# Optimization experiments

Hardware: AMD Instinct MI355X
Metric: run time of the kernel (lower is better)

The kernel has to match this reference:

```python
import jax, jax.numpy as jnp
import numpy as np

H = 8            # heads
M = 256          # num_landmarks
PINV_ITERS = 6
PAD = 16         # residual_conv_kernel(33)//2


def layernorm(x, g, b, eps=1e-5):
    mu = x.mean(-1, keepdims=True)
    var = ((x - mu) ** 2).mean(-1, keepdims=True)
    return (x - mu) * jax.lax.rsqrt(var + eps) * g + b


def moore_penrose_pinv(x, iters=PINV_ITERS):
    # iterative Moore-Penrose pseudo-inverse (Nystromformer)
    abs_x = jnp.abs(x)
    col = abs_x.sum(-1)
    row = abs_x.sum(-2)
    z = jnp.swapaxes(x, -1, -2) / (jnp.max(col) * jnp.max(row))
    eye = jnp.eye(x.shape[-1], dtype=x.dtype)
    for _ in range(iters):
        xz = x @ z
        z = 0.25 * z @ (13.0 * eye - xz @ (15.0 * eye - xz @ (7.0 * eye - xz)))
    return z


def attn_block(y, ln1_g, ln1_b, w_qkv, w_out, b_out, res_w,
               ln2_g, ln2_b, w1, b1, w2, b2):
    B, N, D = y.shape
    inner = w_qkv.shape[1] // 3
    dh = inner // H
    xn = layernorm(y, ln1_g, ln1_b)
    qkv = xn @ w_qkv                      # [B,N,3*inner]
    q, k, v = jnp.split(qkv, 3, axis=-1)
    to_heads = lambda t: t.reshape(B, N, H, dh).transpose(0, 2, 1, 3)  # [B,H,N,dh]
    q, k, v = map(to_heads, (q, k, v))
    q = q * (dh ** -0.5)
    l = N // M                            # tokens per landmark (N % M == 0 here)
    q_l = q.reshape(B, H, M, l, dh).mean(3)  # sum/l == mean -> [B,H,M,dh]
    k_l = k.reshape(B, H, M, l, dh).mean(3)
    attn1 = jax.nn.softmax(jnp.einsum('bhnd,bhmd->bhnm', q, k_l), axis=-1)
    attn2 = jax.nn.softmax(jnp.einsum('bhid,bhjd->bhij', q_l, k_l), axis=-1)
    attn3 = jax.nn.softmax(jnp.einsum('bhmd,bhnd->bhmn', q_l, k), axis=-1)
    attn2_inv = moore_penrose_pinv(attn2)
    out = (attn1 @ attn2_inv) @ (attn3 @ v)   # [B,H,N,dh]
    # depthwise residual conv over sequence dim: v as NCHW with C=H, Hdim=N, Wdim=dh
    res = jax.lax.conv_general_dilated(
        v, res_w, window_strides=(1, 1), padding=[(PAD, PAD), (0, 0)],
        dimension_numbers=('NCHW', 'OIHW', 'NCHW'), feature_group_count=H)
    out = out + res
    out = out.transpose(0, 2, 1, 3).reshape(B, N, inner)
    y = y + out @ w_out + b_out
    yn = layernorm(y, ln2_g, ln2_b)
    hdn = jax.nn.gelu(yn @ w1 + b1, approximate=False)
    return y + hdn @ w2 + b2


def setup_inputs() -> dict:
    key = jax.random.key(0)
    ks = jax.random.split(key, 8)
    B, N, D, NB = 4, 4096, 256, 2
    inner = D
    p = lambda k, shp: jax.random.normal(k, shp, jnp.float32) * 0.02
    return {
        'x': jax.random.normal(ks[0], (B, N, D), jnp.float32),
        'ln1_g': jnp.ones((NB, D), jnp.float32),
        'ln1_b': jnp.zeros((NB, D), jnp.float32),
        'w_qkv': p(ks[1], (NB, D, 3 * inner)),
        'w_out': p(ks[2], (NB, inner, D)),
        'b_out': jnp.zeros((NB, D), jnp.float32),
        'res_w': p(ks[3], (NB, H, 1, 33, 1)),
        'ln2_g': jnp.ones((NB, D), jnp.float32),
        'ln2_b': jnp.zeros((NB, D), jnp.float32),
        'w1': p(ks[4], (NB, D, 2 * D)),
        'b1': jnp.zeros((NB, 2 * D), jnp.float32),
        'w2': p(ks[5], (NB, 2 * D, D)),
        'b2': jnp.zeros((NB, D), jnp.float32),
    }


def reference(x, ln1_g, ln1_b, w_qkv, w_out, b_out, res_w,
              ln2_g, ln2_b, w1, b1, w2, b2):
    y = x
    for i in range(ln1_g.shape[0]):
        y = attn_block(y, ln1_g[i], ln1_b[i], w_qkv[i], w_out[i], b_out[i],
                       res_w[i], ln2_g[i], ln2_b[i], w1[i], b1[i], w2[i], b2[i])
    return y
```

## Files before the change

### kernel.cpp

```cpp
#include <hip/hip_runtime.h>
#include <math.h>

typedef float f32x4 __attribute__((ext_vector_type(4)));
typedef short s16x8 __attribute__((ext_vector_type(8)));
typedef unsigned short u16;
typedef unsigned int u32;

#define MFMA16(a,b,c) __builtin_amdgcn_mfma_f32_16x16x32_bf16((a),(b),(c),0,0,0)
#define AS1 __attribute__((address_space(1)))
#define AS3 __attribute__((address_space(3)))

__device__ __forceinline__ void dma16(const u16* g, u16* l){
  __builtin_amdgcn_global_load_lds((const AS1 u32*)g, (AS3 u32*)l, 16, 0, 0);
}

__device__ __forceinline__ float bf2f(u16 u){
  union { unsigned int i; float f; } v; v.i = ((unsigned int)u)<<16; return v.f;
}
__device__ __forceinline__ u16 f2bf(float f){
  union { float f; unsigned int i; } v; v.f = f;
  unsigned int x = v.i;
  return (u16)((x + 0x7fffu + ((x>>16)&1u))>>16);
}

enum { EPI_QKV=0, EPI_BIAS_GELU=3 };

template<int EPI>
__global__ __launch_bounds__(256)
void kgemm2(const u16* __restrict__ A, const u16* __restrict__ BT, int K, int lda, int ldb,
            const float* __restrict__ bias, u16* __restrict__ outb, int ldc,
            u16* __restrict__ qo, u16* __restrict__ ko, u16* __restrict__ vo,
            u16* __restrict__ qlm, u16* __restrict__ klm)
{
  __shared__ __align__(16) u16 As[128*32];
  __shared__ __align__(16) u16 Bs[128*32];
  const int tid = threadIdx.x;
  const int w = tid>>6, wy = w>>1, wx = w&1, l = tid&63, q = l>>4, ln = l&15;
  const int m0 = blockIdx.x*128, n0 = blockIdx.y*128;
  const int lrow = l>>2, lch = l&3;

  f32x4 acc[4][4];
  #pragma unroll
  for (int i=0;i<4;i++)
    #pragma unroll
    for (int j=0;j<4;j++){ acc[i][j][0]=0.f; acc[i][j][1]=0.f; acc[i][j][2]=0.f; acc[i][j][3]=0.f; }

  for (int k0=0; k0<K; k0+=32){
    #pragma unroll
    for (int c=0;c<2;c++){
      int row = 32*w + 16*c + lrow;
      int gch = lch ^ ((row>>1)&3);
      dma16(A + (long)(m0+row)*lda + k0 + gch*8, &As[(32*w+16*c)*32]);
      dma16(BT + (long)(n0+row)*ldb + k0 + gch*8, &Bs[(32*w+16*c)*32]);
    }
    __syncthreads();
    s16x8 af[4], bfr[4];
    #pragma unroll
    for (int mt=0;mt<4;mt++){
      int row = wy*64 + mt*16 + ln;
      af[mt] = *(const s16x8*)&As[row*32 + ((q ^ ((row>>1)&3))<<3)];
    }
    #pragma unroll
    for (int nt=0;nt<4;nt++){
      int row = wx*64 + nt*16 + ln;
      bfr[nt] = *(const s16x8*)&Bs[row*32 + ((q ^ ((row>>1)&3))<<3)];
    }
    #pragma unroll
    for (int mt=0;mt<4;mt++)
      #pragma unroll
      for (int nt=0;nt<4;nt++)
        acc[mt][nt] = MFMA16(af[mt], bfr[nt], acc[mt][nt]);
    __syncthreads();
  }

  #pragma unroll
  for (int mt=0;mt<4;mt++)
  #pragma unroll
  for (int nt=0;nt<4;nt++){
    int ncol = n0 + wx*64 + nt*16 + ln;
    if (EPI==EPI_QKV){
      int sel = ncol>>8, hd = ncol&255, h = hd>>5, d = hd&31;
      u16* dst = sel==0 ? qo : (sel==1 ? ko : vo);
      float sc2 = (sel==0) ? 0.17677669529663689f : 1.f;
      float s = 0.f;
      #pragma unroll
      for (int r=0;r<4;r++){
        int mrow = m0 + wy*64 + mt*16 + q*4 + r;
        int b = mrow>>12, n = mrow&4095;
        float v = acc[mt][nt][r]*sc2;
        dst[(((long)(b*8+h)*4096 + n)<<5) + d] = f2bf(v);
        s += v;
      }
      if (sel < 2){
        s += __shfl_xor(s, 16);
        s += __shfl_xor(s, 32);
        if (q == 0){
          int mrow0 = m0 + wy*64 + mt*16;
          int b = mrow0>>12, grp = (mrow0&4095)>>4;
          u16* ldst = (sel==0) ? qlm : klm;
          ldst[(((long)(b*8+h)*256 + grp)<<5) + d] = f2bf(s*(1.0f/16.0f));
        }
      }
    } else {
      #pragma unroll
      for (int r=0;r<4;r++){
        int mrow = m0 + wy*64 + mt*16 + q*4 + r;
        float x = acc[mt][nt][r] + bias[ncol];
        float g = 0.5f*x*(1.0f + erff(x*0.70710678118654752f));
        outb[(long)mrow*ldc + ncol] = f2bf(g);
      }
    }
  }
}

__global__ __launch_bounds__(256)
void kgemmLN(const u16* __restrict__ A, const u16* __restrict__ BT, int K,
             const float* __restrict__ bias, const float* __restrict__ base,
             float* __restrict__ yout,
             const float* __restrict__ lng, const float* __restrict__ lnb,
             u16* __restrict__ xnout)
{
  __shared__ __align__(16) u16 As[64*32];
  __shared__ __align__(16) u16 Bs[256*32];
  __shared__ float red[64][4];
  const int tid = threadIdx.x;
  const int w = tid>>6, l = tid&63, q = l>>4, ln = l&15;
  const int m0 = blockIdx.x*64;

  f32x4 acc[4][4];
  #pragma unroll
  for (int i=0;i<4;i++)
    #pragma unroll
    for (int j=0;j<4;j++){ acc[i][j][0]=0.f; acc[i][j][1]=0.f; acc[i][j][2]=0.f; acc[i][j][3]=0.f; }

  for (int k0=0; k0<K; k0+=32){
    {
      int row = w*16 + (l>>2);
      int gch = (l&3) ^ ((row>>1)&3);
      dma16(A + (long)(m0+row)*K + k0 + gch*8, &As[(w*16)*32]);
    }
    #pragma unroll
    for (int c=0;c<4;c++){
      int row = c*64 + w*16 + (l>>2);
      int gch = (l&3) ^ ((row>>1)&3);
      dma16(BT + (long)row*K + k0 + gch*8, &Bs[(c*64+w*16)*32]);
    }
    __syncthreads();
    s16x8 af[4], bfr[4];
    #pragma unroll
    for (int mt=0;mt<4;mt++){
      int row = mt*16 + ln;
      af[mt] = *(const s16x8*)&As[row*32 + ((q ^ ((row>>1)&3))<<3)];
    }
    #pragma unroll
    for (int nt=0;nt<4;nt++){
      int row = w*64 + nt*16 + ln;
      bfr[nt] = *(const s16x8*)&Bs[row*32 + ((q ^ ((row>>1)&3))<<3)];
    }
    #pragma unroll
    for (int mt=0;mt<4;mt++)
      #pragma unroll
      for (int nt=0;nt<4;nt++)
        acc[mt][nt] = MFMA16(af[mt], bfr[nt], acc[mt][nt]);
    __syncthreads();
  }

  float rb[4];
  #pragma unroll
  for (int nt=0;nt<4;nt++) rb[nt] = bias[w*64 + nt*16 + ln];
  #pragma unroll
  for (int mt=0;mt<4;mt++)
  #pragma unroll
  for (int r=0;r<4;r++){
    long rowb = (long)(m0 + mt*16 + q*4 + r)*256;
    #pragma unroll
    for (int nt=0;nt<4;nt++){
      int col = w*64 + nt*16 + ln;
      float v = base[rowb + col] + acc[mt][nt][r] + rb[nt];
      acc[mt][nt][r] = v;
      yout[rowb + col] = v;
    }
  }
  #pragma unroll
  for (int mt=0;mt<4;mt++)
  #pragma unroll
  for (int r=0;r<4;r++){
    float s = acc[mt][0][r]+acc[mt][1][r]+acc[mt][2][r]+acc[mt][3][r];
    s += __shfl_xor(s,1); s += __shfl_xor(s,2); s += __shfl_xor(s,4); s += __shfl_xor(s,8);
    if (ln==0) red[mt*16+q*4+r][w] = s;
  }
  __syncthreads();
  float mu[4][4];
  #pragma unroll
  for (int mt=0;mt<4;mt++)
  #pragma unroll
  for (int r=0;r<4;r++){
    int row = mt*16+q*4+r;
    mu[mt][r] = (red[row][0]+red[row][1]+red[row][2]+red[row][3])*(1.0f/256.0f);
  }
  __syncthreads();
  #pragma unroll
  for (int mt=0;mt<4;mt++)
  #pragma unroll
  for (int r=0;r<4;r++){
    float vs = 0.f;
    #pragma unroll
    for (int nt=0;nt<4;nt++){ float d = acc[mt][nt][r]-mu[mt][r]; vs += d*d; }
    vs += __shfl_xor(vs,1); vs += __shfl_xor(vs,2); vs += __shfl_xor(vs,4); vs += __shfl_xor(vs,8);
    if (ln==0) red[mt*16+q*4+r][w] = vs;
  }
  __syncthreads();
  float rg[4], rbb[4];
  #pragma unroll
  for (int nt=0;nt<4;nt++){ int col = w*64+nt*16+ln; rg[nt]=lng[col]; rbb[nt]=lnb[col]; }
  #pragma unroll
  for (int mt=0;mt<4;mt++)
  #pragma unroll
  for (int r=0;r<4;r++){
    int row = mt*16+q*4+r;
    float rs = rsqrtf((red[row][0]+red[row][1]+red[row][2]+red[row][3])*(1.0f/256.0f) + 1e-5f);
    long rowb = (long)(m0 + row)*256;
    #pragma unroll
    for (int nt=0;nt<4;nt++){
      int col = w*64 + nt*16 + ln;
      float d = acc[mt][nt][r]-mu[mt][r];
      xnout[rowb + col] = f2bf(d*rs*rg[nt] + rbb[nt]);
    }
  }
}

__device__ __forceinline__ int swidx(int row, int col){
  int cc = col>>3;
  int sl = (cc&24)|((cc&7)^((row>>1)&7));
  return row*256 + sl*8 + (col&7);
}
__device__ __forceinline__ int slot8(int ca, int row){
  return ((ca&24)|((ca&7)^((row>>1)&7)))<<3;
}

__device__ __forceinline__ void stage256(const u16* __restrict__ g, u16* lds, int w, int l){
  const int drow = l>>5, dch = l&31;
  #pragma unroll
  for (int c=0;c<16;c++){
    int base = (c*8 + w)*2;
    int row = base + drow;
    int gch = (dch&24) | ((dch&7) ^ ((row>>1)&7));
    dma16(g + (long)row*256 + gch*8, &lds[base*256]);
  }
}
__device__ __forceinline__ void stage32(const u16* __restrict__ g, u16* lds, int w, int l){
  const int drow = l>>5, dch = l&31;
  #pragma unroll
  for (int c=0;c<2;c++){
    int base = (c*8 + w)*2;
    int row = base + drow;
    int gch = (dch&24) | ((dch&7) ^ ((row>>1)&7));
    dma16(g + (long)row*256 + gch*8, &lds[base*256]);
  }
}
__device__ __forceinline__ void stage16(const u16* __restrict__ g, u16* lds, int w, int l){
  const int drow = l>>5, dch = l&31;
  int row = w*2 + drow;
  int gch = (dch&24) | ((dch&7) ^ ((row>>1)&7));
  dma16(g + (long)row*256 + gch*8, &lds[(w*2)*256]);
}

__device__ __forceinline__ void loadBf(const u16* bL, int w, int l, s16x8 (&bw)[2][8]){
  const int q=l>>4, ln=l&15, wn0=w*32;
  #pragma unroll
  for (int nt=0;nt<2;nt++)
    #pragma unroll
    for (int kq=0;kq<8;kq++){
      int n = wn0 + nt*16 + ln, ca = kq*4+q;
      bw[nt][kq] = *(const s16x8*)&bL[n*256 + slot8(ca, n)];
    }
}

__device__ __forceinline__ void multAr(const u16* aL, int arow0, const s16x8 (&bw)[2][8],
                                       int l, f32x4 (&acc)[2][2]){
  const int q=l>>4, ln=l&15;
  #pragma unroll
  for (int mt=0;mt<2;mt++)
    #pragma unroll
    for (int nt=0;nt<2;nt++){ acc[mt][nt][0]=0.f; acc[mt][nt][1]=0.f; acc[mt][nt][2]=0.f; acc[mt][nt][3]=0.f; }
  #pragma unroll
  for (int kq=0;kq<8;kq++){
    int ca = kq*4+q;
    s16x8 af[2];
    #pragma unroll
    for (int mt=0;mt<2;mt++){
      int r = arow0 + mt*16 + ln;
      af[mt] = *(const s16x8*)&aL[r*256 + slot8(ca, r)];
    }
    #pragma unroll
    for (int mt=0;mt<2;mt++)
      #pragma unroll
      for (int nt=0;nt<2;nt++)
        acc[mt][nt] = MFMA16(af[mt], bw[nt][kq], acc[mt][nt]);
  }
}

__device__ __forceinline__ void multHr(const u16* hL, const s16x8 (&bw)[2][8],
                                       int l, f32x4 (&hacc)[2]){
  const int q=l>>4, ln=l&15;
  hacc[0][0]=0.f; hacc[0][1]=0.f; hacc[0][2]=0.f; hacc[0][3]=0.f;
  hacc[1][0]=0.f; hacc[1][1]=0.f; hacc[1][2]=0.f; hacc[1][3]=0.f;
  #pragma unroll
  for (int kq=0;kq<8;kq++){
    int ca = kq*4+q;
    s16x8 af = *(const s16x8*)&hL[ln*256 + slot8(ca, ln)];
    hacc[0] = MFMA16(af, bw[0][kq], hacc[0]);
    hacc[1] = MFMA16(af, bw[1][kq], hacc[1]);
  }
}

__device__ __forceinline__ void polyinit13(const u16* aL, int arow0, int w, int l, f32x4 (&poly)[2][2]){
  const int q=l>>4, ln=l&15, wn0=w*32;
  #pragma unroll
  for (int mt=0;mt<2;mt++)
  #pragma unroll
  for (int nt=0;nt<2;nt++)
  #pragma unroll
  for (int r=0;r<4;r++){
    int row = arow0 + mt*16 + q*4 + r;
    int col = wn0 + nt*16 + ln;
    poly[mt][nt][r] = 13.f*bf2f(aL[swidx(row,col)]);
  }
}
__device__ __forceinline__ void init13H(const u16* hL, int w, int l, f32x4 (&hpoly)[2]){
  const int q=l>>4, ln=l&15, wn0=w*32;
  #pragma unroll
  for (int nt=0;nt<2;nt++)
  #pragma unroll
  for (int r=0;r<4;r++)
    hpoly[nt][r] = 13.f*bf2f(hL[swidx(q*4+r, wn0+nt*16+ln)]);
}
__device__ __forceinline__ void polyaxpy(f32x4 (&poly)[2][2], const f32x4 (&acc)[2][2], float sc){
  #pragma unroll
  for (int mt=0;mt<2;mt++)
    #pragma unroll
    for (int nt=0;nt<2;nt++)
      #pragma unroll
      for (int r=0;r<4;r++) poly[mt][nt][r] += sc*acc[mt][nt][r];
}
__device__ __forceinline__ void axpyH(f32x4 (&hpoly)[2], const f32x4 (&hacc)[2], float sc){
  #pragma unroll
  for (int nt=0;nt<2;nt++)
    #pragma unroll
    for (int r=0;r<4;r++) hpoly[nt][r] += sc*hacc[nt][r];
}
__device__ __forceinline__ void writeT(u16* Ts, const f32x4 (&acc)[2][2], int w, int l, float sc){
  const int q=l>>4, ln=l&15, wn0=w*32;
  #pragma unroll
  for (int mt=0;mt<2;mt++)
  #pragma unroll
  for (int nt=0;nt<2;nt++)
  #pragma unroll
  for (int r=0;r<4;r++){
    int row = mt*16 + q*4 + r;
    int col = wn0 + nt*16 + ln;
    Ts[swidx(row,col)] = f2bf(sc*acc[mt][nt][r]);
  }
}
__device__ __forceinline__ void writeH(u16* Hs, const f32x4 (&hacc)[2], int w, int l){
  const int q=l>>4, ln=l&15, wn0=w*32;
  #pragma unroll
  for (int nt=0;nt<2;nt++)
  #pragma unroll
  for (int r=0;r<4;r++)
    Hs[swidx(q*4+r, wn0+nt*16+ln)] = f2bf(hacc[nt][r]);
}
__device__ __forceinline__ void epi_poly(u16* __restrict__ out, int rowbase,
                                         const f32x4 (&poly)[2][2], int w, int l, float sc){
  const int q=l>>4, ln=l&15, wn0=w*32;
  #pragma unroll
  for (int mt=0;mt<2;mt++)
  #pragma unroll
  for (int nt=0;nt<2;nt++)
  #pragma unroll
  for (int r=0;r<4;r++){
    int row = rowbase + mt*16 + q*4 + r;
    int col = wn0 + nt*16 + ln;
    out[(long)row*256 + col] = f2bf(sc*poly[mt][nt][r]);
  }
}
__device__ __forceinline__ void epiH(u16* __restrict__ out, const f32x4 (&hpoly)[2],
                                     int w, int l, float sc){
  const int q=l>>4, ln=l&15, wn0=w*32;
  #pragma unroll
  for (int nt=0;nt<2;nt++)
  #pragma unroll
  for (int r=0;r<4;r++)
    out[(long)(q*4+r)*256 + wn0+nt*16+ln] = f2bf(sc*hpoly[nt][r]);
}

__device__ __forceinline__ void mult32(const u16* aL, int arow0, const u16* bL,
                                       int w, int l, f32x4 (&acc)[2][2]){
  const int q=l>>4, ln=l&15, wn0=w*32;
  #pragma unroll
  for (int mt=0;mt<2;mt++)
    #pragma unroll
    for (int nt=0;nt<2;nt++){ acc[mt][nt][0]=0.f; acc[mt][nt][1]=0.f; acc[mt][nt][2]=0.f; acc[mt][nt][3]=0.f; }
  #pragma unroll
  for (int kq=0;kq<8;kq++){
    int ca = kq*4+q;
    s16x8 af[2];
    #pragma unroll
    for (int mt=0;mt<2;mt++){
      int r = arow0 + mt*16 + ln;
      af[mt] = *(const s16x8*)&aL[r*256 + slot8(ca,r)];
    }
    #pragma unroll
    for (int nt=0;nt<2;nt++){
      int n = wn0 + nt*16 + ln;
      s16x8 bfr = *(const s16x8*)&bL[n*256 + slot8(ca,n)];
      acc[0][nt] = MFMA16(af[0], bfr, acc[0][nt]);
      acc[1][nt] = MFMA16(af[1], bfr, acc[1][nt]);
    }
  }
}

__global__ __launch_bounds__(512)
void kw0(const float* __restrict__ cs_p, float* __restrict__ scal,
         const float* __restrict__ num_p, const float* __restrict__ den_p,
         const u16* __restrict__ X, u16* __restrict__ W0, u16* __restrict__ h0)
{
  __shared__ __align__(16) u16 Wf[65536];
  __shared__ __align__(16) u16 Ts[8192];
  const int tid=threadIdx.x, w=tid>>6, l=tid&63;
  const int bid=blockIdx.x, xcd=bid&7, j=bid>>3;
  const int batch = xcd*4 + (j>>3), slab = j&7;

  stage256(X + (long)batch*65536, Wf, w, l);

  float* red = (float*)Ts;
  float mx = 0.f;
  for (int i=tid;i<8192;i+=512){
    float s = 0.f;
    #pragma unroll
    for (int c=0;c<8;c++) s += cs_p[(long)c*8192 + i];
    mx = fmaxf(mx, s);
  }
  red[tid] = mx; __syncthreads();
  for (int s=256;s>0;s>>=1){ if (tid<s) red[tid] = fmaxf(red[tid], red[tid+s]); __syncthreads(); }
  float s0 = 1.0f/red[0];
  if (bid==0 && tid==0) scal[0] = s0;

  f32x4 acc[2][2];
  mult32(Wf, slab*32, Wf, w, l, acc);
  {
    const int q=l>>4, ln=l&15, wn0=w*32;
    u16* ob = W0 + (long)batch*65536;
    #pragma unroll
    for (int mt=0;mt<2;mt++)
    #pragma unroll
    for (int nt=0;nt<2;nt++)
    #pragma unroll
    for (int r=0;r<4;r++){
      int row = slab*32 + mt*16 + q*4 + r;
      int col = wn0 + nt*16 + ln;
      ob[(long)row*256 + col] = f2bf(acc[mt][nt][r]*s0);
    }
  }

  if (slab==0){
    __syncthreads();
    float (*lt)[257] = (float(*)[257])Wf;
    for (int i=tid;i<8192;i+=512){
      int m = i>>5, d = i&31;
      float sn = 0.f, sd = 0.f;
      #pragma unroll
      for (int c=0;c<8;c++){
        sn += num_p[((long)(c*32+batch))*8192 + i];
        sd += den_p[(c*32+batch)*256 + m];
      }
      lt[d][m] = sn/sd;
    }
    __syncthreads();
    u16* o = h0 + (long)batch*8192;
    for (int j2=tid;j2<8192;j2+=512){
      int d = j2>>8, m = j2&255;
      o[j2] = f2bf(lt[d][m]);
    }
  }
}

__global__ __launch_bounds__(512)
void kiter(const u16* __restrict__ Win, u16* __restrict__ Wout,
           const u16* __restrict__ hin, u16* __restrict__ hout)
{
  __shared__ __align__(16) u16 Wf[65536];
  __shared__ __align__(16) u16 Ts[8192];
  __shared__ __align__(16) u16 Hs[4096];
  const int tid=threadIdx.x, w=tid>>6, l=tid&63;
  const int bid=blockIdx.x, xcd=bid&7, j=bid>>3;
  const int batch = xcd*4 + (j>>3), slab = j&7;
  const bool hrole = (slab&3)==0;
  const int hr0 = (slab>>2)*16;

  stage256(Win + (long)batch*65536, Wf, w, l);
  if (hrole) stage16(hin + (long)batch*8192 + hr0*256, Hs, w, l);
  __syncthreads();

  s16x8 bw[2][8];
  loadBf(Wf, w, l, bw);

  f32x4 acc[2][2], poly[2][2];
  f32x4 hacc[2], hpoly[2];

  polyinit13(Wf, slab*32, w, l, poly);
  multAr(Wf, slab*32, bw, l, acc);
  polyaxpy(poly, acc, -15.f);
  if (hrole){
    init13H(Hs, w, l, hpoly);
    multHr(Hs, bw, l, hacc);
    axpyH(hpoly, hacc, -15.f);
  }
  __syncthreads();
  writeT(Ts, acc, w, l, 1.f);
  if (hrole) writeH(Hs, hacc, w, l);
  __syncthreads();
  multAr(Ts, 0, bw, l, acc);
  polyaxpy(poly, acc, 7.f);
  if (hrole){ multHr(Hs, bw, l, hacc); axpyH(hpoly, hacc, 7.f); }
  __syncthreads();
  writeT(Ts, acc, w, l, 1.f);
  if (hrole) writeH(Hs, hacc, w, l);
  __syncthreads();
  multAr(Ts, 0, bw, l, acc);
  polyaxpy(poly, acc, -1.f);
  epi_poly(Wout + (long)batch*65536, slab*32, poly, w, l, 0.25f);
  if (hrole){
    multHr(Hs, bw, l, hacc);
    axpyH(hpoly, hacc, -1.f);
    epiH(hout + (long)batch*8192 + hr0*256, hpoly, w, l, 0.25f);
  }
}

__global__ __launch_bounds__(512)
void ktail(const u16* __restrict__ W5, const u16* __restrict__ h5,
           const u16* __restrict__ XT, const float* __restrict__ scal,
           u16* __restrict__ uT)
{
  __shared__ __align__(16) u16 Wf[65536];
  __shared__ __align__(16) u16 Ts[8192];
  const int tid=threadIdx.x, w=tid>>6, l=tid&63;
  const int batch = blockIdx.x;

  stage256(W5 + (long)batch*65536, Wf, w, l);
  stage32(h5 + (long)batch*8192, Ts, w, l);
  __syncthreads();

  s16x8 bw[2][8];
  loadBf(Wf, w, l, bw);

  f32x4 acc[2][2], poly[2][2];
  polyinit13(Ts, 0, w, l, poly);
  multAr(Ts, 0, bw, l, acc);
  polyaxpy(poly, acc, -15.f);
  __syncthreads(); writeT(Ts, acc, w, l, 1.f); __syncthreads();
  multAr(Ts, 0, bw, l, acc);
  polyaxpy(poly, acc, 7.f);
  __syncthreads(); writeT(Ts, acc, w, l, 1.f); __syncthreads();
  multAr(Ts, 0, bw, l, acc);
  polyaxpy(poly, acc, -1.f);
  __syncthreads();
  writeT(Ts, poly, w, l, 0.25f);
  stage256(XT + (long)batch*65536, Wf, w, l);
  __syncthreads();
  loadBf(Wf, w, l, bw);
  multAr(Ts, 0, bw, l, acc);
  const float s0 = scal[0];
  {
    const int q=l>>4, ln=l&15, wn0=w*32;
    u16* ob = uT + (long)batch*8192;
    #pragma unroll
    for (int mt=0;mt<2;mt++)
    #pragma unroll
    for (int nt=0;nt<2;nt++)
    #pragma unroll
    for (int r=0;r<4;r++){
      int row = mt*16 + q*4 + r;
      int col = wn0 + nt*16 + ln;
      ob[(long)row*256 + col] = f2bf(acc[mt][nt][r]*s0);
    }
  }
}

__global__ __launch_bounds__(256)
void kattn23(const u16* __restrict__ ql, const u16* __restrict__ kl,
             u16* __restrict__ X, u16* __restrict__ XT, float* __restrict__ cs_p,
             const u16* __restrict__ kk, const u16* __restrict__ vv,
             float* __restrict__ num_p, float* __restrict__ den_p)
{
  __shared__ __align__(16) u16 Pbuf[4][64][40];
  __shared__ __align__(16) u16 vT[32][40];
  __shared__ float qrow[32][33];
  __shared__ float psum[32][4];
  __shared__ float rsum[32];
  int bh = blockIdx.y;
  int tid = threadIdx.x, w = tid>>6, l = tid&63, q = l>>4, ln = l&15;

  if (blockIdx.x < 8){
    int r0 = blockIdx.x*32;
    int c = tid;
    #pragma unroll
    for (int i=0;i<4;i++){
      int e = c*4+i; int rr = e>>5, dd = e&31;
      qrow[rr][dd] = bf2f(ql[((long)bh*256 + r0+rr)*32 + dd]);
    }
    float kc[32];
    {
      const u16* kp = kl + ((long)bh*256 + c)*32;
      #pragma unroll
      for (int d=0;d<32;d++) kc[d] = bf2f(kp[d]);
    }
    __syncthreads();
    float er[32]; float colacc = 0.f;
    for (int r=0;r<32;r++){
      float s = 0.f;
      #pragma unroll
      for (int d=0;d<32;d++) s += qrow[r][d]*kc[d];
      float e = __expf(s);
      er[r] = e;
      float wsum = e;
      #pragma unroll
      for (int m=1;m<64;m<<=1) wsum += __shfl_xor(wsum, m);
      if (l==0) psum[r][w] = wsum;
    }
    __syncthreads();
    if (c<32) rsum[c] = psum[c][0]+psum[c][1]+psum[c][2]+psum[c][3];
    __syncthreads();
    for (int r=0;r<32;r++){
      float x = er[r]/rsum[r];
      u16 xb = f2bf(x);
      X [((long)bh*256 + r0+r)*256 + c] = xb;
      XT[((long)bh*256 + c)*256 + r0+r] = xb;
      colacc += x;
    }
    cs_p[(long)blockIdx.x*8192 + bh*256 + c] = colacc;
    return;
  }

  int chunk = blockIdx.x - 8;
  f32x4 z4; z4[0]=0.f; z4[1]=0.f; z4[2]=0.f; z4[3]=0.f;
  f32x4 acc[4][2]; f32x4 dacc[4];
  #pragma unroll
  for (int mt=0;mt<4;mt++){ dacc[mt]=z4; acc[mt][0]=z4; acc[mt][1]=z4; }
  const u16* qlb = ql + (long)bh*8192;
  const u16* kb  = kk + (long)bh*131072;
  const u16* vb  = vv + (long)bh*131072;
  int vn = tid>>3, vd = (tid&7)*4;
  for (int s=0;s<16;s++){
    int n0 = chunk*512 + s*32;
    ushort4 vx = *(const ushort4*)(vb + (long)(n0+vn)*32 + vd);
    vT[vd+0][vn]=vx.x; vT[vd+1][vn]=vx.y; vT[vd+2][vn]=vx.z; vT[vd+3][vn]=vx.w;
    __syncthreads();
    s16x8 bk[2];
    #pragma unroll
    for (int nt=0;nt<2;nt++) bk[nt] = *(const s16x8*)(kb + (long)(n0 + nt*16 + ln)*32 + q*8);
    #pragma unroll
    for (int mt=0;mt<4;mt++){
      s16x8 aq = *(const s16x8*)(qlb + (long)(w*64 + mt*16 + ln)*32 + q*8);
      #pragma unroll
      for (int nt=0;nt<2;nt++){
        f32x4 sf = MFMA16(aq, bk[nt], z4);
        f32x4 ef;
        #pragma unroll
        for (int r=0;r<4;r++) ef[r] = __expf(sf[r]);
        dacc[mt] += ef;
        #pragma unroll
        for (int r=0;r<4;r++) Pbuf[w][mt*16 + q*4 + r][nt*16 + ln] = f2bf(ef[r]);
      }
    }
    #pragma unroll
    for (int mt=0;mt<4;mt++){
      s16x8 ap = *(const s16x8*)&Pbuf[w][mt*16 + ln][q*8];
      #pragma unroll
      for (int nt=0;nt<2;nt++){
        s16x8 bv = *(const s16x8*)&vT[nt*16 + ln][q*8];
        acc[mt][nt] = MFMA16(ap, bv, acc[mt][nt]);
      }
    }
    __syncthreads();
  }
  #pragma unroll
  for (int mt=0;mt<4;mt++)
    #pragma unroll
    for (int r=0;r<4;r++){
      float x = dacc[mt][r];
      x += __shfl_xor(x,1); x += __shfl_xor(x,2); x += __shfl_xor(x,4); x += __shfl_xor(x,8);
      dacc[mt][r] = x;
    }
  long pbase = (long)(chunk*32 + bh);
  #pragma unroll
  for (int mt=0;mt<4;mt++)
    #pragma unroll
    for (int nt=0;nt<2;nt++)
      #pragma unroll
      for (int r=0;r<4;r++){
        int mg = w*64 + mt*16 + q*4 + r;
        num_p[pbase*8192 + (long)mg*32 + nt*16 + ln] = acc[mt][nt][r];
      }
  if (ln==0){
    #pragma unroll
    for (int mt=0;mt<4;mt++)
      #pragma unroll
      for (int r=0;r<4;r++)
        den_p[pbase*256 + w*64 + mt*16 + q*4 + r] = dacc[mt][r];
  }
}

__global__ __launch_bounds__(256)
void kattn1u(const u16* __restrict__ qq, const u16* __restrict__ kl, const u16* __restrict__ uT,
             const u16* __restrict__ vv, const float* __restrict__ rw,
             u16* __restrict__ aoutb)
{
  int nch = blockIdx.x, bh = blockIdx.y;
  int b = bh>>3, h = bh&7;
  int tid = threadIdx.x, w = tid>>6, l = tid&63, q = l>>4, ln = l&15;
  __shared__ __align__(16) u16 Pbuf[4][32][40];
  __shared__ __align__(16) u16 vtile[160][36];
  int r0g = nch*128;
  const u16* vb = vv + (long)bh*131072;
  #pragma unroll
  for (int it=0; it<5; it++){
    int slot = tid + it*256;
    int rr = slot>>3, c = (slot&7)*4;
    int s = r0g - 16 + rr;
    ushort4 val; val.x=0; val.y=0; val.z=0; val.w=0;
    if (s>=0 && s<4096) val = *(const ushort4*)(vb + (long)s*32 + c);
    *(ushort4*)&vtile[rr][c] = val;
  }
  __syncthreads();

  f32x4 z4; z4[0]=0.f; z4[1]=0.f; z4[2]=0.f; z4[3]=0.f;
  f32x4 acc[2][2]; f32x4 dacc[2];
  #pragma unroll
  for (int mt=0;mt<2;mt++){ dacc[mt]=z4; acc[mt][0]=z4; acc[mt][1]=z4; }
  const u16* qb  = qq + (long)bh*131072;
  const u16* klb = kl + (long)bh*8192;
  const u16* ub  = uT + (long)bh*8192;
  int r0 = r0g + w*32;
  for (int s=0;s<8;s++){
    s16x8 bk[2];
    #pragma unroll
    for (int nt=0;nt<2;nt++) bk[nt] = *(const s16x8*)(klb + (long)(s*32 + nt*16 + ln)*32 + q*8);
    #pragma unroll
    for (int mt=0;mt<2;mt++){
      s16x8 aq = *(const s16x8*)(qb + (long)(r0 + mt*16 + ln)*32 + q*8);
      #pragma unroll
      for (int nt=0;nt<2;nt++){
        f32x4 sf = MFMA16(aq, bk[nt], z4);
        f32x4 ef;
        #pragma unroll
        for (int r=0;r<4;r++) ef[r] = __expf(sf[r]);
        dacc[mt] += ef;
        #pragma unroll
        for (int r=0;r<4;r++) Pbuf[w][mt*16 + q*4 + r][nt*16 + ln] = f2bf(ef[r]);
      }
    }
    #pragma unroll
    for (int mt=0;mt<2;mt++){
      s16x8 ap = *(const s16x8*)&Pbuf[w][mt*16 + ln][q*8];
      #pragma unroll
      for (int nt=0;nt<2;nt++){
        s16x8 bu = *(const s16x8*)(ub + (long)(nt*16 + ln)*256 + s*32 + q*8);
        acc[mt][nt] = MFMA16(ap, bu, acc[mt][nt]);
      }
    }
  }
  #pragma unroll
  for (int mt=0;mt<2;mt++)
    #pragma unroll
    for (int r=0;r<4;r++){
      float x = dacc[mt][r];
      x += __shfl_xor(x,1); x += __shfl_xor(x,2); x += __shfl_xor(x,4); x += __shfl_xor(x,8);
      dacc[mt][r] = x;
    }

  const float* wp = rw + h*33;
  float w_[33];
  #pragma unroll
  for (int j=0;j<33;j++) w_[j] = wp[j];

  #pragma unroll
  for (int mt=0;mt<2;mt++){
    int nl = w*32 + mt*16 + q*4;
    #pragma unroll
    for (int nt=0;nt<2;nt++){
      int d = nt*16 + ln;
      float vvv[36];
      #pragma unroll
      for (int j=0;j<36;j++) vvv[j] = bf2f(vtile[nl + j][d]);
      #pragma unroll
      for (int r=0;r<4;r++){
        float cv = 0.f;
        #pragma unroll
        for (int j=0;j<33;j++) cv += w_[j]*vvv[r+j];
        int n = r0 + mt*16 + q*4 + r;
        long oidx = ((long)b*4096 + n)*256 + h*32 + d;
        aoutb[oidx] = f2bf(acc[mt][nt][r]/dacc[mt][r] + cv);
      }
    }
  }
}

__global__ __launch_bounds__(256)
void kcvtln(const float* __restrict__ xin, const float* __restrict__ lg, const float* __restrict__ lb,
            u16* __restrict__ xn,
            const float* __restrict__ wqkv, const float* __restrict__ wout,
            const float* __restrict__ w1, const float* __restrict__ w2,
            u16* __restrict__ wqkvT, u16* __restrict__ woutT,
            u16* __restrict__ w1T, u16* __restrict__ w2T)
{
  __shared__ float t[32][33];
  int z = blockIdx.x;
  if (z < 4096){
    int w = threadIdx.x>>6, l = threadIdx.x&63;
    long row = (long)z*4 + w;
    float4 v = ((const float4*)(xin + row*256))[l];
    float s = v.x+v.y+v.z+v.w;
    #pragma unroll
    for (int m=1;m<64;m<<=1) s += __shfl_xor(s, m);
    float mu = s*(1.0f/256.0f);
    float dx=v.x-mu, dy=v.y-mu, dz=v.z-mu, dw=v.w-mu;
    float s2 = dx*dx+dy*dy+dz*dz+dw*dw;
    #pragma unroll
    for (int m=1;m<64;m<<=1) s2 += __shfl_xor(s2, m);
    float rs = rsqrtf(s2*(1.0f/256.0f) + 1e-5f);
    float4 gg = ((const float4*)lg)[l];
    float4 bb = ((const float4*)lb)[l];
    ushort4 o;
    o.x = f2bf(dx*rs*gg.x + bb.x);
    o.y = f2bf(dy*rs*gg.y + bb.y);
    o.z = f2bf(dz*rs*gg.z + bb.z);
    o.w = f2bf(dw*rs*gg.w + bb.w);
    *(ushort4*)(xn + row*256 + l*4) = o;
    return;
  }
  z -= 4096;
  const float* src; u16* dst; int K, Nn, bx, by;
  if (z < 384){      int i=z/192, r=z%192; src=wqkv+(long)i*196608; dst=wqkvT+(long)i*196608; K=256; Nn=768; bx=r%24; by=r/24; }
  else if (z < 512){ int zz=z-384; int i=zz/64, r=zz%64; src=wout+(long)i*65536; dst=woutT+(long)i*65536; K=256; Nn=256; bx=r%8; by=r/8; }
  else if (z < 768){ int zz=z-512; int i=zz/128, r=zz%128; src=w1+(long)i*131072; dst=w1T+(long)i*131072; K=256; Nn=512; bx=r%16; by=r/16; }
  else {             int zz=z-768; int i=zz/128, r=zz%128; src=w2+(long)i*131072; dst=w2T+(long)i*131072; K=512; Nn=256; bx=r%8; by=r/8; }
  int n0 = bx*32, k0 = by*32;
  int tx = threadIdx.x&31, ty = threadIdx.x>>5;
  #pragma unroll
  for (int i=0;i<4;i++) t[ty+i*8][tx] = src[(long)(k0+ty+i*8)*Nn + n0+tx];
  __syncthreads();
  #pragma unroll
  for (int i=0;i<4;i++) dst[(long)(n0+ty+i*8)*K + k0+tx] = f2bf(t[tx][ty+i*8]);
}

extern "C" void kernel_launch(void* const* d_in, const int* in_sizes, int n_in,
                              void* d_out, int out_size, void* d_ws, size_t ws_size,
                              hipStream_t stream)
{
  const float* x    = (const float*)d_in[0];
  const float* ln1g = (const float*)d_in[1];
  const float* ln1b = (const float*)d_in[2];
  const float* wqkv = (const float*)d_in[3];
  const float* wout = (const float*)d_in[4];
  const float* bout = (const float*)d_in[5];
  const float* resw = (const float*)d_in[6];
  const float* ln2g = (const float*)d_in[7];
  const float* ln2b = (const float*)d_in[8];
  const float* w1   = (const float*)d_in[9];
  const float* b1   = (const float*)d_in[10];
  const float* w2   = (const float*)d_in[11];
  const float* b2   = (const float*)d_in[12];
  float* y = (float*)d_out;
  char* ws = (char*)d_ws;

  u16* xn    = (u16*)(ws + 0);
  u16* qb    = (u16*)(ws + 8388608);
  u16* kb    = (u16*)(ws + 16777216);
  u16* vb    = (u16*)(ws + 25165824);
  u16* ql    = (u16*)(ws + 33554432);
  u16* kl    = (u16*)(ws + 34078720);
  u16* X     = (u16*)(ws + 34603008);
  u16* XT    = (u16*)(ws + 38797312);
  u16* h0b   = (u16*)(ws + 42991616);
  u16* WA    = (u16*)(ws + 51380224);
  u16* WB    = (u16*)(ws + 55574528);
  u16* hA    = (u16*)(ws + 68157440);
  u16* hB    = (u16*)(ws + 72351744);
  float* num_p = (float*)(ws + 76546048);
  float* den_p = (float*)(ws + 84934656);
  float* cs_p  = (float*)(ws + 85196800);
  float* scal  = (float*)(ws + 85458944);
  u16* uT    = (u16*)(ws + 85459200);
  u16* aoutb = (u16*)(ws + 85983488);
  u16* wqkvT = (u16*)(ws + 94372096);
  u16* woutT = (u16*)(ws + 95158528);
  u16* w1T   = (u16*)(ws + 95420672);
  u16* w2T   = (u16*)(ws + 95944960);
  u16* hdn   = (u16*)(ws + 51380224);

  (void)in_sizes; (void)n_in; (void)out_size; (void)ws_size;

  kcvtln<<<5120,256,0,stream>>>(x, ln1g, ln1b, xn,
      wqkv, wout, w1, w2, wqkvT, woutT, w1T, w2T);

  for (int i=0;i<2;i++){
    kgemm2<EPI_QKV><<<dim3(128,6),256,0,stream>>>(xn, wqkvT + (long)i*196608, 256, 256, 256,
        nullptr, nullptr, 0, qb,kb,vb, ql,kl);
    kattn23<<<dim3(16,32),256,0,stream>>>(ql, kl, X, XT, cs_p, kb, vb, num_p, den_p);

    kw0<<<256,512,0,stream>>>(cs_p, scal, num_p, den_p, X, WA, h0b);
    u16 *Wi = WA, *Wo = WB, *hi = h0b, *ho = hA;
    for (int it=0; it<5; it++){
      kiter<<<256,512,0,stream>>>(Wi, Wo, hi, ho);
      u16* t = Wi; Wi = Wo; Wo = t;
      hi = ho; ho = (ho == hA) ? hB : hA;
    }
    ktail<<<32,512,0,stream>>>(Wi, hi, XT, scal, uT);

    kattn1u<<<dim3(32,32),256,0,stream>>>(qb, kl, uT, vb, resw + i*264, aoutb);
    kgemmLN<<<256,256,0,stream>>>(aoutb, woutT + (long)i*65536, 256,
        bout + i*256, i==0 ? x : y, y, ln2g + i*256, ln2b + i*256, xn);
    kgemm2<EPI_BIAS_GELU><<<dim3(128,4),256,0,stream>>>(xn, w1T + (long)i*131072, 256, 256, 256,
        b1 + i*512, hdn, 512, nullptr,nullptr,nullptr, nullptr,nullptr);
    kgemmLN<<<256,256,0,stream>>>(hdn, w2T + (long)i*131072, 512,
        b2 + i*256, y, y, ln1g + 256, ln1b + 256, xn);
  }
}
```

Measured before the change: 501.6 us.

## Load pinv operands from global directly, double-buffer V tiles, hoist Q fragments

The Newton-Schulz pinv kernels (kw0, kiter, kfinal) no longer stage the full 256x256 bf16 matrix into a 128KB LDS buffer. They read MFMA fragments straight from global memory, which drops the staging barriers and lets more blocks fit per CU. The landmark attention kernel gets a double-buffered transposed V tile with a register prefetch, so one barrier per step is removed. The Q fragment loads are hoisted out of the loop in two kernels, and kattn1u stores its conv tile transposed so the reads are vectorized. The tradeoff is more global and L2 traffic from repeated fragment reads and higher register pressure.

```diff
diff --git a/kernel.cpp b/kernel.cpp
--- a/kernel.cpp
+++ b/kernel.cpp
@@ -238,42 +238,36 @@
   return ((ca&24)|((ca&7)^((row>>1)&7)))<<3;
 }
 
-__device__ __forceinline__ void stage256(const u16* __restrict__ g, u16* lds, int w, int l){
-  const int drow = l>>5, dch = l&31;
-  #pragma unroll
-  for (int c=0;c<16;c++){
-    int base = (c*8 + w)*2;
-    int row = base + drow;
-    int gch = (dch&24) | ((dch&7) ^ ((row>>1)&7));
-    dma16(g + (long)row*256 + gch*8, &lds[base*256]);
-  }
-}
-__device__ __forceinline__ void stage32(const u16* __restrict__ g, u16* lds, int w, int l){
-  const int drow = l>>5, dch = l&31;
-  #pragma unroll
-  for (int c=0;c<2;c++){
-    int base = (c*8 + w)*2;
-    int row = base + drow;
-    int gch = (dch&24) | ((dch&7) ^ ((row>>1)&7));
-    dma16(g + (long)row*256 + gch*8, &lds[base*256]);
-  }
-}
-__device__ __forceinline__ void stage16(const u16* __restrict__ g, u16* lds, int w, int l){
-  const int drow = l>>5, dch = l&31;
-  int row = w*2 + drow;
-  int gch = (dch&24) | ((dch&7) ^ ((row>>1)&7));
-  dma16(g + (long)row*256 + gch*8, &lds[(w*2)*256]);
-}
-
-__device__ __forceinline__ void loadBf(const u16* bL, int w, int l, s16x8 (&bw)[2][8]){
+__device__ __forceinline__ void loadBfG(const u16* __restrict__ g, int w, int l, s16x8 (&bw)[2][8]){
   const int q=l>>4, ln=l&15, wn0=w*32;
   #pragma unroll
   for (int nt=0;nt<2;nt++)
     #pragma unroll
     for (int kq=0;kq<8;kq++){
-      int n = wn0 + nt*16 + ln, ca = kq*4+q;
-      bw[nt][kq] = *(const s16x8*)&bL[n*256 + slot8(ca, n)];
-    }
+      int n = wn0 + nt*16 + ln;
+      bw[nt][kq] = *(const s16x8*)(g + (long)n*256 + (kq*4+q)*8);
+    }
+}
+
+__device__ __forceinline__ void multArG(const u16* __restrict__ Ag, int arow0,
+                                        const s16x8 (&bw)[2][8], int l, f32x4 (&acc)[2][2]){
+  const int q=l>>4, ln=l&15;
+  #pragma unroll
+  for (int mt=0;mt<2;mt++)
+    #pragma unroll
+    for (int nt=0;nt<2;nt++){ acc[mt][nt][0]=0.f; acc[mt][nt][1]=0.f; acc[mt][nt][2]=0.f; acc[mt][nt][3]=0.f; }
+  #pragma unroll
+  for (int kq=0;kq<8;kq++){
+    s16x8 af[2];
+    #pragma unroll
+    for (int mt=0;mt<2;mt++)
+      af[mt] = *(const s16x8*)(Ag + (long)(arow0+mt*16+ln)*256 + (kq*4+q)*8);
+    #pragma unroll
+    for (int mt=0;mt<2;mt++)
+      #pragma unroll
+      for (int nt=0;nt<2;nt++)
+        acc[mt][nt] = MFMA16(af[mt], bw[nt][kq], acc[mt][nt]);
+  }
 }
 
 __device__ __forceinline__ void multAr(const u16* aL, int arow0, const s16x8 (&bw)[2][8],
@@ -297,6 +291,19 @@
       #pragma unroll
       for (int nt=0;nt<2;nt++)
         acc[mt][nt] = MFMA16(af[mt], bw[nt][kq], acc[mt][nt]);
+  }
+}
+
+__device__ __forceinline__ void multHrG(const u16* __restrict__ Hg, const s16x8 (&bw)[2][8],
+                                        int l, f32x4 (&hacc)[2]){
+  const int q=l>>4, ln=l&15;
+  hacc[0][0]=0.f; hacc[0][1]=0.f; hacc[0][2]=0.f; hacc[0][3]=0.f;
+  hacc[1][0]=0.f; hacc[1][1]=0.f; hacc[1][2]=0.f; hacc[1][3]=0.f;
+  #pragma unroll
+  for (int kq=0;kq<8;kq++){
+    s16x8 af = *(const s16x8*)(Hg + (long)ln*256 + (kq*4+q)*8);
+    hacc[0] = MFMA16(af, bw[0][kq], hacc[0]);
+    hacc[1] = MFMA16(af, bw[1][kq], hacc[1]);
   }
 }
 
@@ -314,26 +321,24 @@
   }
 }
 
-__device__ __forceinline__ void polyinit13(const u16* aL, int arow0, int w, int l, f32x4 (&poly)[2][2]){
+__device__ __forceinline__ void polyinit13G(const u16* __restrict__ Ag, int arow0,
+                                            int w, int l, f32x4 (&poly)[2][2]){
   const int q=l>>4, ln=l&15, wn0=w*32;
   #pragma unroll
   for (int mt=0;mt<2;mt++)
   #pragma unroll
   for (int nt=0;nt<2;nt++)
   #pragma unroll
-  for (int r=0;r<4;r++){
-    int row = arow0 + mt*16 + q*4 + r;
-    int col = wn0 + nt*16 + ln;
-    poly[mt][nt][r] = 13.f*bf2f(aL[swidx(row,col)]);
-  }
-}
-__device__ __forceinline__ void init13H(const u16* hL, int w, int l, f32x4 (&hpoly)[2]){
+  for (int r=0;r<4;r++)
+    poly[mt][nt][r] = 13.f*bf2f(Ag[(long)(arow0+mt*16+q*4+r)*256 + wn0+nt*16+ln]);
+}
+__device__ __forceinline__ void init13HG(const u16* __restrict__ Hg, int w, int l, f32x4 (&hpoly)[2]){
   const int q=l>>4, ln=l&15, wn0=w*32;
   #pragma unroll
   for (int nt=0;nt<2;nt++)
   #pragma unroll
   for (int r=0;r<4;r++)
-    hpoly[nt][r] = 13.f*bf2f(hL[swidx(q*4+r, wn0+nt*16+ln)]);
+    hpoly[nt][r] = 13.f*bf2f(Hg[(long)(q*4+r)*256 + wn0+nt*16+ln]);
 }
 __device__ __forceinline__ void polyaxpy(f32x4 (&poly)[2][2], const f32x4 (&acc)[2][2], float sc){
   #pragma unroll
@@ -392,32 +397,6 @@
   #pragma unroll
   for (int r=0;r<4;r++)
     out[(long)(q*4+r)*256 + wn0+nt*16+ln] = f2bf(sc*hpoly[nt][r]);
-}
-
-__device__ __forceinline__ void mult32(const u16* aL, int arow0, const u16* bL,
-                                       int w, int l, f32x4 (&acc)[2][2]){
-  const int q=l>>4, ln=l&15, wn0=w*32;
-  #pragma unroll
-  for (int mt=0;mt<2;mt++)
-    #pragma unroll
-    for (int nt=0;nt<2;nt++){ acc[mt][nt][0]=0.f; acc[mt][nt][1]=0.f; acc[mt][nt][2]=0.f; acc[mt][nt][3]=0.f; }
-  #pragma unroll
-  for (int kq=0;kq<8;kq++){
-    int ca = kq*4+q;
-    s16x8 af[2];
-    #pragma unroll
-    for (int mt=0;mt<2;mt++){
-      int r = arow0 + mt*16 + ln;
-      af[mt] = *(const s16x8*)&aL[r*256 + slot8(ca,r)];
-    }
-    #pragma unroll
-    for (int nt=0;nt<2;nt++){
-      int n = wn0 + nt*16 + ln;
-      s16x8 bfr = *(const s16x8*)&bL[n*256 + slot8(ca,n)];
-      acc[0][nt] = MFMA16(af[0], bfr, acc[0][nt]);
-      acc[1][nt] = MFMA16(af[1], bfr, acc[1][nt]);
-    }
-  }
 }
 
 __global__ __launch_bounds__(512)
@@ -425,15 +404,16 @@
          const float* __restrict__ num_p, const float* __restrict__ den_p,
          const u16* __restrict__ X, u16* __restrict__ W0, u16* __restrict__ h0)
 {
-  __shared__ __align__(16) u16 Wf[65536];
-  __shared__ __align__(16) u16 Ts[8192];
+  __shared__ __align__(16) char sm[33024];
   const int tid=threadIdx.x, w=tid>>6, l=tid&63;
   const int bid=blockIdx.x, xcd=bid&7, j=bid>>3;
   const int batch = xcd*4 + (j>>3), slab = j&7;
-
-  stage256(X + (long)batch*65536, Wf, w, l);
-
-  float* red = (float*)Ts;
+  const u16* Xg = X + (long)batch*65536;
+
+  s16x8 bw[2][8];
+  loadBfG(Xg, w, l, bw);
+
+  float* red = (float*)sm;
   float mx = 0.f;
   for (int i=tid;i<8192;i+=512){
     float s = 0.f;
@@ -447,7 +427,7 @@
   if (bid==0 && tid==0) scal[0] = s0;
 
   f32x4 acc[2][2];
-  mult32(Wf, slab*32, Wf, w, l, acc);
+  multArG(Xg, slab*32, bw, l, acc);
   {
     const int q=l>>4, ln=l&15, wn0=w*32;
     u16* ob = W0 + (long)batch*65536;
@@ -465,7 +445,7 @@
 
   if (slab==0){
     __syncthreads();
-    float (*lt)[257] = (float(*)[257])Wf;
+    float (*lt)[257] = (float(*)[257])sm;
     for (int i=tid;i<8192;i+=512){
       int m = i>>5, d = i&31;
       float sn = 0.f, sd = 0.f;
@@ -489,7 +469,6 @@
 void kiter(const u16* __restrict__ Win, u16* __restrict__ Wout,
            const u16* __restrict__ hin, u16* __restrict__ hout)
 {
-  __shared__ __align__(16) u16 Wf[65536];
   __shared__ __align__(16) u16 Ts[8192];
   __shared__ __align__(16) u16 Hs[4096];
   const int tid=threadIdx.x, w=tid>>6, l=tid&63;
@@ -497,26 +476,23 @@
   const int batch = xcd*4 + (j>>3), slab = j&7;
   const bool hrole = (slab&3)==0;
   const int hr0 = (slab>>2)*16;
-
-  stage256(Win + (long)batch*65536, Wf, w, l);
-  if (hrole) stage16(hin + (long)batch*8192 + hr0*256, Hs, w, l);
-  __syncthreads();
+  const u16* Wg = Win + (long)batch*65536;
+  const u16* Hg = hin + (long)batch*8192 + hr0*256;
 
   s16x8 bw[2][8];
-  loadBf(Wf, w, l, bw);
+  loadBfG(Wg, w, l, bw);
 
   f32x4 acc[2][2], poly[2][2];
   f32x4 hacc[2], hpoly[2];
 
-  polyinit13(Wf, slab*32, w, l, poly);
-  multAr(Wf, slab*32, bw, l, acc);
+  polyinit13G(Wg, slab*32, w, l, poly);
+  multArG(Wg, slab*32, bw, l, acc);
   polyaxpy(poly, acc, -15.f);
   if (hrole){
-    init13H(Hs, w, l, hpoly);
-    multHr(Hs, bw, l, hacc);
+    init13HG(Hg, w, l, hpoly);
+    multHrG(Hg, bw, l, hacc);
     axpyH(hpoly, hacc, -15.f);
   }
-  __syncthreads();
   writeT(Ts, acc, w, l, 1.f);
   if (hrole) writeH(Hs, hacc, w, l);
   __syncthreads();
@@ -542,33 +518,32 @@
            const u16* __restrict__ XT, const float* __restrict__ scal,
            u16* __restrict__ uT)
 {
-  __shared__ __align__(16) u16 Wf[65536];
   __shared__ __align__(16) u16 Ts[8192];
   const int tid=threadIdx.x, w=tid>>6, l=tid&63;
   const int batch = blockIdx.x;
-
-  stage256(W5 + (long)batch*65536, Wf, w, l);
-  stage32(h5 + (long)batch*8192, Ts, w, l);
-  __syncthreads();
+  const u16* Wg = W5 + (long)batch*65536;
+  const u16* Hg = h5 + (long)batch*8192;
 
   s16x8 bw[2][8];
-  loadBf(Wf, w, l, bw);
+  loadBfG(Wg, w, l, bw);
 
   f32x4 acc[2][2], poly[2][2];
-  polyinit13(Ts, 0, w, l, poly);
-  multAr(Ts, 0, bw, l, acc);
+  polyinit13G(Hg, 0, w, l, poly);
+  multArG(Hg, 0, bw, l, acc);
   polyaxpy(poly, acc, -15.f);
-  __syncthreads(); writeT(Ts, acc, w, l, 1.f); __syncthreads();
+  writeT(Ts, acc, w, l, 1.f);
+  __syncthreads();
   multAr(Ts, 0, bw, l, acc);
   polyaxpy(poly, acc, 7.f);
-  __syncthreads(); writeT(Ts, acc, w, l, 1.f); __syncthreads();
+  __syncthreads();
+  writeT(Ts, acc, w, l, 1.f);
+  __syncthreads();
   multAr(Ts, 0, bw, l, acc);
   polyaxpy(poly, acc, -1.f);
+  loadBfG(XT + (long)batch*65536, w, l, bw);
   __syncthreads();
   writeT(Ts, poly, w, l, 0.25f);
-  stage256(XT + (long)batch*65536, Wf, w, l);
-  __syncthreads();
-  loadBf(Wf, w, l, bw);
+  __syncthreads();
   multAr(Ts, 0, bw, l, acc);
   const float s0 = scal[0];
   {
@@ -594,7 +569,7 @@
              float* __restrict__ num_p, float* __restrict__ den_p)
 {
   __shared__ __align__(16) u16 Pbuf[4][64][40];
-  __shared__ __align__(16) u16 vT[32][40];
+  __shared__ __align__(16) u16 vT2[2][32][40];
   __shared__ float qrow[32][33];
   __shared__ float psum[32][4];
   __shared__ float rsum[32];
@@ -650,21 +625,28 @@
   const u16* qlb = ql + (long)bh*8192;
   const u16* kb  = kk + (long)bh*131072;
   const u16* vb  = vv + (long)bh*131072;
+  s16x8 aq[4];
+  #pragma unroll
+  for (int mt=0;mt<4;mt++) aq[mt] = *(const s16x8*)(qlb + (long)(w*64 + mt*16 + ln)*32 + q*8);
   int vn = tid>>3, vd = (tid&7)*4;
+  {
+    ushort4 vx = *(const ushort4*)(vb + (long)(chunk*512+vn)*32 + vd);
+    vT2[0][vd+0][vn]=vx.x; vT2[0][vd+1][vn]=vx.y; vT2[0][vd+2][vn]=vx.z; vT2[0][vd+3][vn]=vx.w;
+  }
+  __syncthreads();
   for (int s=0;s<16;s++){
+    int cur = s&1;
+    ushort4 vnx;
+    if (s<15) vnx = *(const ushort4*)(vb + (long)(chunk*512+(s+1)*32+vn)*32 + vd);
     int n0 = chunk*512 + s*32;
-    ushort4 vx = *(const ushort4*)(vb + (long)(n0+vn)*32 + vd);
-    vT[vd+0][vn]=vx.x; vT[vd+1][vn]=vx.y; vT[vd+2][vn]=vx.z; vT[vd+3][vn]=vx.w;
-    __syncthreads();
     s16x8 bk[2];
     #pragma unroll
     for (int nt=0;nt<2;nt++) bk[nt] = *(const s16x8*)(kb + (long)(n0 + nt*16 + ln)*32 + q*8);
     #pragma unroll
     for (int mt=0;mt<4;mt++){
-      s16x8 aq = *(const s16x8*)(qlb + (long)(w*64 + mt*16 + ln)*32 + q*8);
       #pragma unroll
       for (int nt=0;nt<2;nt++){
-        f32x4 sf = MFMA16(aq, bk[nt], z4);
+        f32x4 sf = MFMA16(aq[mt], bk[nt], z4);
         f32x4 ef;
         #pragma unroll
         for (int r=0;r<4;r++) ef[r] = __expf(sf[r]);
@@ -678,9 +660,13 @@
       s16x8 ap = *(const s16x8*)&Pbuf[w][mt*16 + ln][q*8];
       #pragma unroll
       for (int nt=0;nt<2;nt++){
-        s16x8 bv = *(const s16x8*)&vT[nt*16 + ln][q*8];
+        s16x8 bv = *(const s16x8*)&vT2[cur][nt*16 + ln][q*8];
         acc[mt][nt] = MFMA16(ap, bv, acc[mt][nt]);
       }
+    }
+    if (s<15){
+      int nxt = cur^1;
+      vT2[nxt][vd+0][vn]=vnx.x; vT2[nxt][vd+1][vn]=vnx.y; vT2[nxt][vd+2][vn]=vnx.z; vT2[nxt][vd+3][vn]=vnx.w;
     }
     __syncthreads();
   }
@@ -720,7 +706,7 @@
   int b = bh>>3, h = bh&7;
   int tid = threadIdx.x, w = tid>>6, l = tid&63, q = l>>4, ln = l&15;
   __shared__ __align__(16) u16 Pbuf[4][32][40];
-  __shared__ __align__(16) u16 vtile[160][36];
+  __shared__ __align__(16) u16 vtileT[32][164];
   int r0g = nch*128;
   const u16* vb = vv + (long)bh*131072;
   #pragma unroll
@@ -730,7 +716,7 @@
     int s = r0g - 16 + rr;
     ushort4 val; val.x=0; val.y=0; val.z=0; val.w=0;
     if (s>=0 && s<4096) val = *(const ushort4*)(vb + (long)s*32 + c);
-    *(ushort4*)&vtile[rr][c] = val;
+    vtileT[c+0][rr]=val.x; vtileT[c+1][rr]=val.y; vtileT[c+2][rr]=val.z; vtileT[c+3][rr]=val.w;
   }
   __syncthreads();
 
@@ -742,16 +728,18 @@
   const u16* klb = kl + (long)bh*8192;
   const u16* ub  = uT + (long)bh*8192;
   int r0 = r0g + w*32;
+  s16x8 aq[2];
+  #pragma unroll
+  for (int mt=0;mt<2;mt++) aq[mt] = *(const s16x8*)(qb + (long)(r0 + mt*16 + ln)*32 + q*8);
   for (int s=0;s<8;s++){
     s16x8 bk[2];
     #pragma unroll
     for (int nt=0;nt<2;nt++) bk[nt] = *(const s16x8*)(klb + (long)(s*32 + nt*16 + ln)*32 + q*8);
     #pragma unroll
     for (int mt=0;mt<2;mt++){
-      s16x8 aq = *(const s16x8*)(qb + (long)(r0 + mt*16 + ln)*32 + q*8);
       #pragma unroll
       for (int nt=0;nt<2;nt++){
-        f32x4 sf = MFMA16(aq, bk[nt], z4);
+        f32x4 sf = MFMA16(aq[mt], bk[nt], z4);
         f32x4 ef;
         #pragma unroll
         for (int r=0;r<4;r++) ef[r] = __expf(sf[r]);
@@ -791,8 +779,13 @@
     for (int nt=0;nt<2;nt++){
       int d = nt*16 + ln;
       float vvv[36];
-      #pragma unroll
-      for (int j=0;j<36;j++) vvv[j] = bf2f(vtile[nl + j][d]);
+      const u16* vp = &vtileT[d][nl];
+      #pragma unroll
+      for (int jj=0;jj<9;jj++){
+        ushort4 vq = *(const ushort4*)(vp + jj*4);
+        vvv[jj*4+0]=bf2f(vq.x); vvv[jj*4+1]=bf2f(vq.y);
+        vvv[jj*4+2]=bf2f(vq.z); vvv[jj*4+3]=bf2f(vq.w);
+      }
       #pragma unroll
       for (int r=0;r<4;r++){
         float cv = 0.f;
```

Result: slower. 586.0 us (+16.8%).
